# Performance work log

Measured on AMD Instinct MI355X. Metric: run time of the kernel, lower is better.

The kernel has to match this reference:

```python
import jax, jax.numpy as jnp
import numpy as np

HIDDEN = 1024
MSG = 1024
T = 3
B = 256
N = 80  # num_categories


def setup_inputs() -> dict:
    key = jax.random.key(0)
    ks = jax.random.split(key, 10)
    s = 0.02
    return {
        "x": jax.random.normal(ks[0], (B, N), dtype=jnp.float32),
        # msg_update_fn: Linear(hidden->msg) + ReLU
        "W1": jax.random.normal(ks[1], (MSG, HIDDEN), dtype=jnp.float32) * s,
        "b1": jax.random.normal(ks[2], (MSG,), dtype=jnp.float32) * s,
        # GRUCell(msg_dim -> hidden_dim), torch layout [3*hidden, in]
        "Wih": jax.random.normal(ks[3], (3 * HIDDEN, MSG), dtype=jnp.float32) * s,
        "Whh": jax.random.normal(ks[4], (3 * HIDDEN, HIDDEN), dtype=jnp.float32) * s,
        "bih": jax.random.normal(ks[5], (3 * HIDDEN,), dtype=jnp.float32) * s,
        "bhh": jax.random.normal(ks[6], (3 * HIDDEN,), dtype=jnp.float32) * s,
        # Conv1d(hidden, 1, kernel=1) == per-position linear projection
        "w_s": jax.random.normal(ks[7], (HIDDEN,), dtype=jnp.float32) * s,
        "b_s": jax.random.normal(ks[8], (), dtype=jnp.float32) * s,
    }


def _gru_cell(msg, h, Wih, Whh, bih, bhh):
    # torch GRUCell: gate order (r, z, n)
    gi = msg @ Wih.T + bih  # [rows, 3H]
    gh = h @ Whh.T + bhh
    i_r, i_z, i_n = jnp.split(gi, 3, axis=-1)
    h_r, h_z, h_n = jnp.split(gh, 3, axis=-1)
    r = jax.nn.sigmoid(i_r + h_r)
    z = jax.nn.sigmoid(i_z + h_z)
    n = jnp.tanh(i_n + r * h_n)
    return (1.0 - z) * n + z * h


def reference(x, W1, b1, Wih, Whh, bih, bhh, w_s, b_s):
    batch, num_cat = x.shape
    pad_left = (HIDDEN - 1) // 2
    # hidden_0: each scalar label embedded at position pad_left of a zero vector
    hidden = jnp.zeros((batch, num_cat, HIDDEN), dtype=x.dtype).at[:, :, pad_left].set(x)
    for _ in range(T):
        m = jax.nn.relu(jnp.einsum("bnh,mh->bnm", hidden, W1) + b1)  # [B,N,MSG]
        # all-pairs masked mean over j != i  ==  (total sum - self) / (N-1)
        msg = (jnp.sum(m, axis=1, keepdims=True) - m) / (num_cat - 1)
        hidden = _gru_cell(
            msg.reshape(-1, MSG), hidden.reshape(-1, HIDDEN), Wih, Whh, bih, bhh
        ).reshape(batch, num_cat, HIDDEN)
    # Conv1d(hidden->1, k=1) over [B, hidden, N] then squeeze -> [B, N]
    return jnp.einsum("bnh,h->bn", hidden, w_s) + b_s
```

## Files before the change

### kernel.cpp

```cpp
#include <hip/hip_runtime.h>
#include <cstdint>
#include <cstddef>

#define HID 1024
#define NB 256
#define NCAT 80
#define ROWS (NB*NCAT)
#define PADL 511

typedef short short8_t __attribute__((ext_vector_type(8)));
typedef float f32x4_t __attribute__((ext_vector_type(4)));
typedef unsigned short u16;
typedef u16 u16x8_t __attribute__((ext_vector_type(8)));
typedef u16 u16x4_t __attribute__((ext_vector_type(4)));
typedef float f32x4v_t __attribute__((ext_vector_type(4)));

typedef const __attribute__((address_space(1))) unsigned int guint_t;
typedef __attribute__((address_space(3))) unsigned int luint_t;

__device__ __forceinline__ void gl_lds16(const void* g, void* l) {
  __builtin_amdgcn_global_load_lds((guint_t*)g, (luint_t*)l, 16, 0, 0);
}

__device__ __forceinline__ u16 f2bf(float f) {
  unsigned u = __float_as_uint(f);
  u += 0x7fffu + ((u >> 16) & 1u);
  return (u16)(u >> 16);
}
__device__ __forceinline__ float bf2f(u16 s) {
  return __uint_as_float(((unsigned)s) << 16);
}

__device__ __forceinline__ f32x4_t mfma16(short8_t a, short8_t b, f32x4_t c) {
  return __builtin_amdgcn_mfma_f32_16x16x32_bf16(a, b, c, 0, 0, 0);
}

__global__ void cvt_w_kernel(const float* __restrict__ W1, const float* __restrict__ Wih,
                             const float* __restrict__ Whh, u16* __restrict__ W1b,
                             u16* __restrict__ Wihb, u16* __restrict__ Whhb) {
  int idx = blockIdx.x * 256 + threadIdx.x;
  const float* src; u16* dst; int off;
  if (idx < 262144) { src = W1; dst = W1b; off = idx; }
  else if (idx < 1048576) { src = Wih; dst = Wihb; off = idx - 262144; }
  else { src = Whh; dst = Whhb; off = idx - 1048576; }
  f32x4v_t v = reinterpret_cast<const f32x4v_t*>(src)[off];
  u16 o0 = f2bf(v[0]), o1 = f2bf(v[1]), o2 = f2bf(v[2]), o3 = f2bf(v[3]);
  u16* d = dst + (size_t)off * 4;
  d[0] = o0; d[1] = o1; d[2] = o2; d[3] = o3;
}

__global__ void m1_kernel(const float* __restrict__ x, const float* __restrict__ W1,
                          const float* __restrict__ b1, u16* __restrict__ mb) {
  long idx = (long)blockIdx.x * 256 + threadIdx.x;
  long e = idx * 8;
  int r = (int)(e >> 10); int c0 = (int)(e & 1023);
  float xv = x[r];
  u16x8_t o;
#pragma unroll
  for (int j = 0; j < 8; j++) {
    int c = c0 + j;
    float v = xv * W1[(size_t)c * 1024 + PADL] + b1[c];
    o[j] = f2bf(v > 0.f ? v : 0.f);
  }
  *reinterpret_cast<u16x8_t*>(mb + e) = o;
}

__global__ void seg_msg_kernel(u16* __restrict__ mb) {
  int b = blockIdx.x;
  int c0 = blockIdx.y * 512 + threadIdx.x * 4;
  u16* base = mb + (size_t)b * (NCAT * 1024) + c0;
  float s0 = 0.f, s1 = 0.f, s2 = 0.f, s3 = 0.f;
#pragma unroll 4
  for (int n = 0; n < NCAT; n++) {
    u16x4_t v = *reinterpret_cast<const u16x4_t*>(base + (size_t)n * 1024);
    s0 += bf2f(v[0]); s1 += bf2f(v[1]); s2 += bf2f(v[2]); s3 += bf2f(v[3]);
  }
  const float inv = 1.0f / (NCAT - 1);
#pragma unroll 4
  for (int n = 0; n < NCAT; n++) {
    u16x4_t v = *reinterpret_cast<const u16x4_t*>(base + (size_t)n * 1024);
    u16x4_t o;
    o[0] = f2bf((s0 - bf2f(v[0])) * inv);
    o[1] = f2bf((s1 - bf2f(v[1])) * inv);
    o[2] = f2bf((s2 - bf2f(v[2])) * inv);
    o[3] = f2bf((s3 - bf2f(v[3])) * inv);
    *reinterpret_cast<u16x4_t*>(base + (size_t)n * 1024) = o;
  }
}

__device__ __forceinline__ void gm_stage(int kb, char* dstbase, const u16* hb,
                                         const u16* W1b, int rb, int nb, int tid) {
#pragma unroll
  for (int i = 0; i < 4; i++) {
    int c = tid + i * 256;
    const u16* src;
    if (c < 512) {
      int r = c >> 2, s = c & 3;
      int sp = s ^ ((r >> 1) & 3);
      src = hb + ((size_t)(rb * 128 + r)) * 1024 + kb * 32 + sp * 8;
    } else {
      int w = c - 512; int r = w >> 2, s = w & 3;
      int sp = s ^ ((r >> 1) & 3);
      src = W1b + ((size_t)(nb * 128 + r)) * 1024 + kb * 32 + sp * 8;
    }
    gl_lds16(src, dstbase + c * 16);
  }
}

__launch_bounds__(256, 4)
__global__ void gemm_m_kernel(const u16* __restrict__ hb, const u16* __restrict__ W1b,
                              const float* __restrict__ b1, u16* __restrict__ mb) {
  __shared__ __attribute__((aligned(128))) char lds[32768];
  const int tid = threadIdx.x;
  const int rb = blockIdx.x, nb = blockIdx.y;
  const int wid = tid >> 6, lane = tid & 63;
  const int wr = wid >> 1, wc = wid & 1;
  const int lr = lane & 15, ls = lane >> 4;
  const int swoff = (ls ^ ((lr >> 1) & 3)) * 16;
  f32x4_t acc[4][4];
  f32x4_t z4 = {0.f, 0.f, 0.f, 0.f};
#pragma unroll
  for (int m2 = 0; m2 < 4; m2++)
#pragma unroll
    for (int n2 = 0; n2 < 4; n2++) acc[m2][n2] = z4;

  gm_stage(0, lds, hb, W1b, rb, nb, tid);
  __syncthreads();
  int cur = 0;
  for (int kb = 0; kb < 32; kb++) {
    char* bc = lds + cur * 16384;
    if (kb + 1 < 32) gm_stage(kb + 1, lds + (cur ^ 1) * 16384, hb, W1b, rb, nb, tid);
    short8_t a[4], bw[4];
#pragma unroll
    for (int m2 = 0; m2 < 4; m2++) {
      int row = wr * 64 + m2 * 16 + lr;
      a[m2] = *reinterpret_cast<const short8_t*>(bc + row * 64 + swoff);
    }
#pragma unroll
    for (int n2 = 0; n2 < 4; n2++) {
      int r = wc * 64 + n2 * 16 + lr;
      bw[n2] = *reinterpret_cast<const short8_t*>(bc + 8192 + r * 64 + swoff);
    }
#pragma unroll
    for (int m2 = 0; m2 < 4; m2++)
#pragma unroll
      for (int n2 = 0; n2 < 4; n2++)
        acc[m2][n2] = mfma16(a[m2], bw[n2], acc[m2][n2]);
    __syncthreads();
    cur ^= 1;
  }
#pragma unroll
  for (int m2 = 0; m2 < 4; m2++)
#pragma unroll
    for (int n2 = 0; n2 < 4; n2++) {
      int col = nb * 128 + wc * 64 + n2 * 16 + lr;
      float bias = b1[col];
#pragma unroll
      for (int j = 0; j < 4; j++) {
        int gr = rb * 128 + wr * 64 + m2 * 16 + ls * 4 + j;
        float v = acc[m2][n2][j] + bias;
        mb[(size_t)gr * 1024 + col] = f2bf(v > 0.f ? v : 0.f);
      }
    }
}

template <int NSEG>
__launch_bounds__(512, 2)
__global__ void gru_kernel(const u16* __restrict__ msgb, const u16* __restrict__ hbin,
                           const u16* __restrict__ Wihb, const u16* __restrict__ Whhb,
                           const float* __restrict__ bih, const float* __restrict__ bhh,
                           const float* __restrict__ x, const float* __restrict__ WhhF,
                           float* __restrict__ hf, u16* __restrict__ hbout) {
  __shared__ __attribute__((aligned(128))) char lds[57344];
  const int tid = threadIdx.x;
  const int rb = blockIdx.x;
  const int hb0 = blockIdx.y * 64;
  const int wid = tid >> 6, lane = tid & 63;
  const int mw = wid >> 1, nw = wid & 1;
  const int lr = lane & 15, ls = lane >> 4;
  const int swoff = (ls ^ ((lr >> 1) & 3)) * 16;

  const int slot = tid & 3;
  const int r0 = tid >> 2;
  const int sp16 = (slot ^ ((r0 >> 1) & 3)) * 16;
  const char* sA0 = (const char*)msgb + ((size_t)(rb * 256 + r0) << 11) + sp16;
  const char* sA1 = (const char*)msgb + ((size_t)(rb * 256 + 128 + r0) << 11) + sp16;
  const int g2 = r0 >> 6, c2 = r0 & 63;
  const char* sW2 = (const char*)Wihb + ((size_t)(g2 * 1024 + hb0 + c2) << 11) + sp16;
  const char* sW3 = (const char*)Wihb + ((size_t)(2048 + hb0 + (r0 & 63)) << 11) + sp16;
  const int d0 = tid * 16, d1 = d0 + 8192, d2 = d0 + 16384, d3 = d0 + 24576;

#define STAGE(BUF) do { \
    gl_lds16(sA0, (BUF) + d0); gl_lds16(sA1, (BUF) + d1); gl_lds16(sW2, (BUF) + d2); \
    if (tid < 256) gl_lds16(sW3, (BUF) + d3); \
    sA0 += 64; sA1 += 64; sW2 += 64; sW3 += 64; } while (0)

  int offA[4], offB[3][2];
#pragma unroll
  for (int m = 0; m < 4; m++) offA[m] = (mw * 64 + m * 16 + lr) * 64 + swoff;
#pragma unroll
  for (int g = 0; g < 3; g++)
#pragma unroll
    for (int n = 0; n < 2; n++)
      offB[g][n] = 16384 + (g * 64 + nw * 32 + n * 16 + lr) * 64 + swoff;

  f32x4_t ar[4][2], az[4][2], an0[4][2], an1[4][2];
  f32x4_t z4 = {0.f, 0.f, 0.f, 0.f};
#pragma unroll
  for (int m = 0; m < 4; m++)
#pragma unroll
    for (int n = 0; n < 2; n++) { ar[m][n] = z4; az[m][n] = z4; an0[m][n] = z4; an1[m][n] = z4; }

#define COMPUTE(BUF, AN) do { \
    short8_t a_[4], bR_[2], bZ_[2], bN_[2]; \
    _Pragma("unroll") for (int m = 0; m < 4; m++) \
      a_[m] = *reinterpret_cast<const short8_t*>((BUF) + offA[m]); \
    _Pragma("unroll") for (int n = 0; n < 2; n++) { \
      bR_[n] = *reinterpret_cast<const short8_t*>((BUF) + offB[0][n]); \
      bZ_[n] = *reinterpret_cast<const short8_t*>((BUF) + offB[1][n]); \
      bN_[n] = *reinterpret_cast<const short8_t*>((BUF) + offB[2][n]); } \
    _Pragma("unroll") for (int m = 0; m < 4; m++) \
    _Pragma("unroll") for (int n = 0; n < 2; n++) { \
      ar[m][n] = mfma16(a_[m], bR_[n], ar[m][n]); \
      az[m][n] = mfma16(a_[m], bZ_[n], az[m][n]); \
      AN[m][n] = mfma16(a_[m], bN_[n], AN[m][n]); } \
  } while (0)

  char* bufA = lds;
  char* bufB = lds + 28672;

  STAGE(bufA);
  __syncthreads();
  for (int kb = 0; kb < 32; kb += 2) {
    STAGE(bufB);
    COMPUTE(bufA, an0);
    __syncthreads();
    if (kb != 30) {
      STAGE(bufA);
    } else if (NSEG == 2) {
      const ptrdiff_t dA = (const char*)hbin - (const char*)msgb - 2048;
      const ptrdiff_t dW = (const char*)Whhb - (const char*)Wihb - 2048;
      sA0 += dA; sA1 += dA; sW2 += dW; sW3 += dW;
      STAGE(bufA);
    }
    COMPUTE(bufB, an0);
    __syncthreads();
  }
  if (NSEG == 2) {
    for (int kb = 0; kb < 32; kb += 2) {
      STAGE(bufB);
      COMPUTE(bufA, an1);
      __syncthreads();
      if (kb != 30) STAGE(bufA);
      COMPUTE(bufB, an1);
      __syncthreads();
    }
  }
#undef STAGE
#undef COMPUTE

#pragma unroll
  for (int n2 = 0; n2 < 2; n2++) {
    int ch = hb0 + nw * 32 + n2 * 16 + lr;
    float br_ = bih[ch] + bhh[ch];
    float bz_ = bih[1024 + ch] + bhh[1024 + ch];
    float bin_ = bih[2048 + ch];
    float bhn_ = bhh[2048 + ch];
    float wr511 = 0.f, wz511 = 0.f, wn511 = 0.f;
    if (NSEG == 1) {
      wr511 = WhhF[(size_t)ch * 1024 + PADL];
      wz511 = WhhF[(size_t)(1024 + ch) * 1024 + PADL];
      wn511 = WhhF[(size_t)(2048 + ch) * 1024 + PADL];
    }
#pragma unroll
    for (int m = 0; m < 4; m++)
#pragma unroll
      for (int j = 0; j < 4; j++) {
        int gr = rb * 256 + mw * 64 + m * 16 + ls * 4 + j;
        float vr = ar[m][n2][j] + br_;
        float vz = az[m][n2][j] + bz_;
        float vin = an0[m][n2][j] + bin_;
        float vhn, hold;
        if (NSEG == 1) {
          float xv = x[gr];
          vr += xv * wr511;
          vz += xv * wz511;
          vhn = xv * wn511 + bhn_;
          hold = (ch == PADL) ? xv : 0.f;
        } else {
          vhn = an1[m][n2][j] + bhn_;
          hold = hf[(size_t)gr * 1024 + ch];
        }
        float rg = 1.f / (1.f + __expf(-vr));
        float zg = 1.f / (1.f + __expf(-vz));
        float ng = tanhf(vin + rg * vhn);
        float hnew = (1.f - zg) * ng + zg * hold;
        hf[(size_t)gr * 1024 + ch] = hnew;
        hbout[(size_t)gr * 1024 + ch] = f2bf(hnew);
      }
  }
}

__global__ void out_proj_kernel(const float* __restrict__ hf, const float* __restrict__ wsv,
                                const float* __restrict__ bs, float* __restrict__ out) {
  int row = blockIdx.x * 4 + (threadIdx.x >> 6);
  int lane = threadIdx.x & 63;
  const float* p = hf + (size_t)row * 1024;
  float s = 0.f;
#pragma unroll
  for (int t = 0; t < 16; t++) s += p[lane + t * 64] * wsv[lane + t * 64];
#pragma unroll
  for (int off = 32; off; off >>= 1) s += __shfl_down(s, off);
  if (lane == 0) out[row] = s + bs[0];
}

extern "C" void kernel_launch(void* const* d_in, const int* in_sizes, int n_in,
                              void* d_out, int out_size, void* d_ws, size_t ws_size,
                              hipStream_t stream) {
  const float* x = (const float*)d_in[0];
  const float* W1 = (const float*)d_in[1];
  const float* b1 = (const float*)d_in[2];
  const float* Wih = (const float*)d_in[3];
  const float* Whh = (const float*)d_in[4];
  const float* bih = (const float*)d_in[5];
  const float* bhh = (const float*)d_in[6];
  const float* wsv = (const float*)d_in[7];
  const float* bs = (const float*)d_in[8];
  float* out = (float*)d_out;

  char* wsp = (char*)d_ws;
  size_t off = 0;
  auto alloc = [&](size_t bytes) { void* p = wsp + off; off += (bytes + 255) & ~(size_t)255; return p; };
  float* hf = (float*)alloc((size_t)ROWS * 1024 * 4);
  u16* hbA = (u16*)alloc((size_t)ROWS * 1024 * 2);
  u16* hbB = (u16*)alloc((size_t)ROWS * 1024 * 2);
  u16* mb = (u16*)alloc((size_t)ROWS * 1024 * 2);
  u16* W1b = (u16*)alloc((size_t)1024 * 1024 * 2);
  u16* Wihb = (u16*)alloc((size_t)3072 * 1024 * 2);
  u16* Whhb = (u16*)alloc((size_t)3072 * 1024 * 2);

  cvt_w_kernel<<<7168, 256, 0, stream>>>(W1, Wih, Whh, W1b, Wihb, Whhb);

  m1_kernel<<<10240, 256, 0, stream>>>(x, W1, b1, mb);
  seg_msg_kernel<<<dim3(NB, 2), 128, 0, stream>>>(mb);
  gru_kernel<1><<<dim3(80, 16), 512, 0, stream>>>(mb, nullptr, Wihb, Whhb, bih, bhh, x, Whh, hf, hbA);

  for (int it = 1; it < 3; it++) {
    u16* hin = (it & 1) ? hbA : hbB;
    u16* hout = (it & 1) ? hbB : hbA;
    gemm_m_kernel<<<dim3(160, 8), 256, 0, stream>>>(hin, W1b, b1, mb);
    seg_msg_kernel<<<dim3(NB, 2), 128, 0, stream>>>(mb);
    gru_kernel<0 + 2><<<dim3(80, 16), 512, 0, stream>>>(mb, hin, Wihb, Whhb, bih, bhh, x, Whh, hf, hout);
  }

  out_proj_kernel<<<5120, 256, 0, stream>>>(hf, wsv, bs, out);
}
```

Baseline: 981.4 us.

## Deepen K-tiles to 64 with prefetch-two pipelining in GEMM and GRU kernels

Both MFMA GEMM kernels now stage K-tiles of 64 elements (128-byte rows with an 8-way XOR swizzle) into two larger LDS buffers. Loads run two tiles ahead, governed by explicit vmcnt waits and raw s_barrier instead of __syncthreads. MFMA sections are wrapped in s_setprio to favour matrix issue. The aim is fewer barriers per K and more load latency hidden, at the cost of doubled LDS per block (64KB and 112KB), which can reduce occupancy.

```diff
diff --git a/kernel.cpp b/kernel.cpp
--- a/kernel.cpp
+++ b/kernel.cpp
@@ -88,35 +88,31 @@
   }
 }
 
-__device__ __forceinline__ void gm_stage(int kb, char* dstbase, const u16* hb,
-                                         const u16* W1b, int rb, int nb, int tid) {
-#pragma unroll
-  for (int i = 0; i < 4; i++) {
-    int c = tid + i * 256;
-    const u16* src;
-    if (c < 512) {
-      int r = c >> 2, s = c & 3;
-      int sp = s ^ ((r >> 1) & 3);
-      src = hb + ((size_t)(rb * 128 + r)) * 1024 + kb * 32 + sp * 8;
-    } else {
-      int w = c - 512; int r = w >> 2, s = w & 3;
-      int sp = s ^ ((r >> 1) & 3);
-      src = W1b + ((size_t)(nb * 128 + r)) * 1024 + kb * 32 + sp * 8;
-    }
-    gl_lds16(src, dstbase + c * 16);
-  }
-}
-
 __launch_bounds__(256, 4)
 __global__ void gemm_m_kernel(const u16* __restrict__ hb, const u16* __restrict__ W1b,
                               const float* __restrict__ b1, u16* __restrict__ mb) {
-  __shared__ __attribute__((aligned(128))) char lds[32768];
+  __shared__ __attribute__((aligned(128))) char lds[65536];
   const int tid = threadIdx.x;
   const int rb = blockIdx.x, nb = blockIdx.y;
   const int wid = tid >> 6, lane = tid & 63;
   const int wr = wid >> 1, wc = wid & 1;
   const int lr = lane & 15, ls = lane >> 4;
-  const int swoff = (ls ^ ((lr >> 1) & 3)) * 16;
+
+  const int r0 = tid >> 3;
+  const int sp16 = (((tid & 7) ^ (r0 & 7)) << 4);
+  const char* sA[4]; const char* sW[4];
+#pragma unroll
+  for (int i = 0; i < 4; i++) {
+    sA[i] = (const char*)hb + ((size_t)(rb * 128 + 32 * i + r0) << 11) + sp16;
+    sW[i] = (const char*)W1b + ((size_t)(nb * 128 + 32 * i + r0) << 11) + sp16;
+  }
+  const int dA0 = tid * 16, dW0 = 16384 + tid * 16;
+
+#define MSTAGE(BUF) do { \
+    _Pragma("unroll") for (int i = 0; i < 4; i++) { gl_lds16(sA[i], (BUF) + dA0 + i * 4096); sA[i] += 128; } \
+    _Pragma("unroll") for (int i = 0; i < 4; i++) { gl_lds16(sW[i], (BUF) + dW0 + i * 4096); sW[i] += 128; } \
+  } while (0)
+
   f32x4_t acc[4][4];
   f32x4_t z4 = {0.f, 0.f, 0.f, 0.f};
 #pragma unroll
@@ -124,31 +120,41 @@
 #pragma unroll
     for (int n2 = 0; n2 < 4; n2++) acc[m2][n2] = z4;
 
-  gm_stage(0, lds, hb, W1b, rb, nb, tid);
-  __syncthreads();
-  int cur = 0;
-  for (int kb = 0; kb < 32; kb++) {
-    char* bc = lds + cur * 16384;
-    if (kb + 1 < 32) gm_stage(kb + 1, lds + (cur ^ 1) * 16384, hb, W1b, rb, nb, tid);
-    short8_t a[4], bw[4];
-#pragma unroll
-    for (int m2 = 0; m2 < 4; m2++) {
-      int row = wr * 64 + m2 * 16 + lr;
-      a[m2] = *reinterpret_cast<const short8_t*>(bc + row * 64 + swoff);
-    }
-#pragma unroll
-    for (int n2 = 0; n2 < 4; n2++) {
-      int r = wc * 64 + n2 * 16 + lr;
-      bw[n2] = *reinterpret_cast<const short8_t*>(bc + 8192 + r * 64 + swoff);
-    }
-#pragma unroll
-    for (int m2 = 0; m2 < 4; m2++)
-#pragma unroll
-      for (int n2 = 0; n2 < 4; n2++)
-        acc[m2][n2] = mfma16(a[m2], bw[n2], acc[m2][n2]);
-    __syncthreads();
-    cur ^= 1;
-  }
+#define MCOMP(BUF, KK) do { \
+    short8_t a_[4], b_[4]; \
+    const int gr_ = ((((KK) * 4 + ls) ^ (lr & 7)) << 4); \
+    _Pragma("unroll") for (int m2 = 0; m2 < 4; m2++) \
+      a_[m2] = *reinterpret_cast<const short8_t*>((BUF) + (wr * 64 + m2 * 16 + lr) * 128 + gr_); \
+    _Pragma("unroll") for (int n2 = 0; n2 < 4; n2++) \
+      b_[n2] = *reinterpret_cast<const short8_t*>((BUF) + 16384 + (wc * 64 + n2 * 16 + lr) * 128 + gr_); \
+    __builtin_amdgcn_s_setprio(1); \
+    _Pragma("unroll") for (int m2 = 0; m2 < 4; m2++) \
+    _Pragma("unroll") for (int n2 = 0; n2 < 4; n2++) \
+      acc[m2][n2] = mfma16(a_[m2], b_[n2], acc[m2][n2]); \
+    __builtin_amdgcn_s_setprio(0); \
+  } while (0)
+
+  MSTAGE(lds);
+  MSTAGE(lds + 32768);
+  asm volatile("s_waitcnt vmcnt(8)" ::: "memory");
+  __builtin_amdgcn_s_barrier();
+
+  for (int t = 0; t < 16; t++) {
+    char* bc = lds + (t & 1) * 32768;
+    MCOMP(bc, 0);
+    MCOMP(bc, 1);
+    __builtin_amdgcn_s_barrier();
+    if (t + 2 < 16) {
+      MSTAGE(bc);
+      asm volatile("s_waitcnt vmcnt(8)" ::: "memory");
+    } else if (t + 2 == 16) {
+      asm volatile("s_waitcnt vmcnt(0)" ::: "memory");
+    }
+    __builtin_amdgcn_s_barrier();
+  }
+#undef MSTAGE
+#undef MCOMP
+
 #pragma unroll
   for (int m2 = 0; m2 < 4; m2++)
 #pragma unroll
@@ -171,38 +177,29 @@
                            const float* __restrict__ bih, const float* __restrict__ bhh,
                            const float* __restrict__ x, const float* __restrict__ WhhF,
                            float* __restrict__ hf, u16* __restrict__ hbout) {
-  __shared__ __attribute__((aligned(128))) char lds[57344];
+  __shared__ __attribute__((aligned(128))) char lds[114688];
   const int tid = threadIdx.x;
   const int rb = blockIdx.x;
   const int hb0 = blockIdx.y * 64;
   const int wid = tid >> 6, lane = tid & 63;
   const int mw = wid >> 1, nw = wid & 1;
   const int lr = lane & 15, ls = lane >> 4;
-  const int swoff = (ls ^ ((lr >> 1) & 3)) * 16;
-
-  const int slot = tid & 3;
-  const int r0 = tid >> 2;
-  const int sp16 = (slot ^ ((r0 >> 1) & 3)) * 16;
-  const char* sA0 = (const char*)msgb + ((size_t)(rb * 256 + r0) << 11) + sp16;
-  const char* sA1 = (const char*)msgb + ((size_t)(rb * 256 + 128 + r0) << 11) + sp16;
-  const int g2 = r0 >> 6, c2 = r0 & 63;
-  const char* sW2 = (const char*)Wihb + ((size_t)(g2 * 1024 + hb0 + c2) << 11) + sp16;
-  const char* sW3 = (const char*)Wihb + ((size_t)(2048 + hb0 + (r0 & 63)) << 11) + sp16;
-  const int d0 = tid * 16, d1 = d0 + 8192, d2 = d0 + 16384, d3 = d0 + 24576;
-
-#define STAGE(BUF) do { \
-    gl_lds16(sA0, (BUF) + d0); gl_lds16(sA1, (BUF) + d1); gl_lds16(sW2, (BUF) + d2); \
-    if (tid < 256) gl_lds16(sW3, (BUF) + d3); \
-    sA0 += 64; sA1 += 64; sW2 += 64; sW3 += 64; } while (0)
-
-  int offA[4], offB[3][2];
-#pragma unroll
-  for (int m = 0; m < 4; m++) offA[m] = (mw * 64 + m * 16 + lr) * 64 + swoff;
+
+  const int r0 = tid >> 3;
+  const int sp16 = (((tid & 7) ^ (r0 & 7)) << 4);
+  const char* sA[4]; const char* sW[3];
+#pragma unroll
+  for (int i = 0; i < 4; i++)
+    sA[i] = (const char*)msgb + ((size_t)(rb * 256 + 64 * i + r0) << 11) + sp16;
 #pragma unroll
   for (int g = 0; g < 3; g++)
-#pragma unroll
-    for (int n = 0; n < 2; n++)
-      offB[g][n] = 16384 + (g * 64 + nw * 32 + n * 16 + lr) * 64 + swoff;
+    sW[g] = (const char*)Wihb + ((size_t)(g * 1024 + hb0 + r0) << 11) + sp16;
+  const int dA0 = tid * 16, dW0 = 32768 + tid * 16;
+
+#define GSTAGE(BUF) do { \
+    _Pragma("unroll") for (int i = 0; i < 4; i++) { gl_lds16(sA[i], (BUF) + dA0 + i * 8192); sA[i] += 128; } \
+    _Pragma("unroll") for (int g = 0; g < 3; g++) { gl_lds16(sW[g], (BUF) + dW0 + g * 8192); sW[g] += 128; } \
+  } while (0)
 
   f32x4_t ar[4][2], az[4][2], an0[4][2], an1[4][2];
   f32x4_t z4 = {0.f, 0.f, 0.f, 0.f};
@@ -211,53 +208,59 @@
 #pragma unroll
     for (int n = 0; n < 2; n++) { ar[m][n] = z4; az[m][n] = z4; an0[m][n] = z4; an1[m][n] = z4; }
 
-#define COMPUTE(BUF, AN) do { \
+#define GCOMP(BUF, KK, AN) do { \
     short8_t a_[4], bR_[2], bZ_[2], bN_[2]; \
+    const int gr_ = ((((KK) * 4 + ls) ^ (lr & 7)) << 4); \
     _Pragma("unroll") for (int m = 0; m < 4; m++) \
-      a_[m] = *reinterpret_cast<const short8_t*>((BUF) + offA[m]); \
+      a_[m] = *reinterpret_cast<const short8_t*>((BUF) + (mw * 64 + m * 16 + lr) * 128 + gr_); \
     _Pragma("unroll") for (int n = 0; n < 2; n++) { \
-      bR_[n] = *reinterpret_cast<const short8_t*>((BUF) + offB[0][n]); \
-      bZ_[n] = *reinterpret_cast<const short8_t*>((BUF) + offB[1][n]); \
-      bN_[n] = *reinterpret_cast<const short8_t*>((BUF) + offB[2][n]); } \
+      const int rr_ = nw * 32 + n * 16 + lr; \
+      bR_[n] = *reinterpret_cast<const short8_t*>((BUF) + 32768 + rr_ * 128 + gr_); \
+      bZ_[n] = *reinterpret_cast<const short8_t*>((BUF) + 32768 + (64 + rr_) * 128 + gr_); \
+      bN_[n] = *reinterpret_cast<const short8_t*>((BUF) + 32768 + (128 + rr_) * 128 + gr_); } \
+    __builtin_amdgcn_s_setprio(1); \
     _Pragma("unroll") for (int m = 0; m < 4; m++) \
     _Pragma("unroll") for (int n = 0; n < 2; n++) { \
       ar[m][n] = mfma16(a_[m], bR_[n], ar[m][n]); \
       az[m][n] = mfma16(a_[m], bZ_[n], az[m][n]); \
       AN[m][n] = mfma16(a_[m], bN_[n], AN[m][n]); } \
+    __builtin_amdgcn_s_setprio(0); \
   } while (0)
 
-  char* bufA = lds;
-  char* bufB = lds + 28672;
-
-  STAGE(bufA);
-  __syncthreads();
-  for (int kb = 0; kb < 32; kb += 2) {
-    STAGE(bufB);
-    COMPUTE(bufA, an0);
-    __syncthreads();
-    if (kb != 30) {
-      STAGE(bufA);
-    } else if (NSEG == 2) {
-      const ptrdiff_t dA = (const char*)hbin - (const char*)msgb - 2048;
-      const ptrdiff_t dW = (const char*)Whhb - (const char*)Wihb - 2048;
-      sA0 += dA; sA1 += dA; sW2 += dW; sW3 += dW;
-      STAGE(bufA);
-    }
-    COMPUTE(bufB, an0);
-    __syncthreads();
-  }
-  if (NSEG == 2) {
-    for (int kb = 0; kb < 32; kb += 2) {
-      STAGE(bufB);
-      COMPUTE(bufA, an1);
-      __syncthreads();
-      if (kb != 30) STAGE(bufA);
-      COMPUTE(bufB, an1);
-      __syncthreads();
-    }
-  }
-#undef STAGE
-#undef COMPUTE
+  GSTAGE(lds);
+  GSTAGE(lds + 57344);
+  asm volatile("s_waitcnt vmcnt(7)" ::: "memory");
+  __builtin_amdgcn_s_barrier();
+
+  const int NT = NSEG * 16;
+  for (int t = 0; t < NT; t++) {
+    char* bc = lds + (t & 1) * 57344;
+    if (NSEG == 2 && t >= 16) {
+      GCOMP(bc, 0, an1);
+      GCOMP(bc, 1, an1);
+    } else {
+      GCOMP(bc, 0, an0);
+      GCOMP(bc, 1, an0);
+    }
+    __builtin_amdgcn_s_barrier();
+    if (t + 2 < NT) {
+      if (NSEG == 2 && t == 14) {
+        const ptrdiff_t jA = (const char*)hbin - (const char*)msgb - 2048;
+        const ptrdiff_t jW = (const char*)Whhb - (const char*)Wihb - 2048;
+#pragma unroll
+        for (int i = 0; i < 4; i++) sA[i] += jA;
+#pragma unroll
+        for (int g = 0; g < 3; g++) sW[g] += jW;
+      }
+      GSTAGE(bc);
+      asm volatile("s_waitcnt vmcnt(7)" ::: "memory");
+    } else if (t + 2 == NT) {
+      asm volatile("s_waitcnt vmcnt(0)" ::: "memory");
+    }
+    __builtin_amdgcn_s_barrier();
+  }
+#undef GSTAGE
+#undef GCOMP
 
 #pragma unroll
   for (int n2 = 0; n2 < 2; n2++) {
@@ -350,7 +353,7 @@
     u16* hout = (it & 1) ? hbB : hbA;
     gemm_m_kernel<<<dim3(160, 8), 256, 0, stream>>>(hin, W1b, b1, mb);
     seg_msg_kernel<<<dim3(NB, 2), 128, 0, stream>>>(mb);
-    gru_kernel<0 + 2><<<dim3(80, 16), 512, 0, stream>>>(mb, hin, Wihb, Whhb, bih, bhh, x, Whh, hf, hout);
+    gru_kernel<2><<<dim3(80, 16), 512, 0, stream>>>(mb, hin, Wihb, Whhb, bih, bhh, x, Whh, hf, hout);
   }
 
   out_proj_kernel<<<5120, 256, 0, stream>>>(hf, wsv, bs, out);
```

New measurement: 2.454 ms. +150.0%, slower.
